# Performance work log

Hardware: AMD Instinct MI355X
Metric: run time of the kernel (lower is better)

## Reference

```python
import jax, jax.numpy as jnp
import numpy as np

# db4 reconstruction filters (pywt convention): rec_lo = reversed(dec_lo),
# rec_hi[k] = (-1)^k * dec_lo[k]
REC_LO = [0.23037781330885523, 0.7148465705525415, 0.6308807679295904,
          -0.02798376941698385, -0.18703481171888114, 0.030841381835986965,
          0.032883011666982945, -0.010597401784997278]
REC_HI = [-0.010597401784997278, -0.032883011666982945, 0.030841381835986965,
          0.18703481171888114, -0.02798376941698385, -0.6308807679295904,
          0.7148465705525415, -0.23037781330885523]
FILT_LEN = 8


def _idwt1d(cA, cD, axis):
    """Periodized single-level inverse DWT along `axis`. N -> 2N."""
    cA = jnp.moveaxis(cA, axis, -1)
    cD = jnp.moveaxis(cD, axis, -1)
    N = cA.shape[-1]
    up_a = jnp.zeros(cA.shape[:-1] + (2 * N,), cA.dtype).at[..., ::2].set(cA)
    up_d = jnp.zeros(cD.shape[:-1] + (2 * N,), cD.dtype).at[..., ::2].set(cD)
    # circular synthesis: y[m] = sum_k g[k]*up_a[m-k] + h[k]*up_d[m-k]
    y = sum(REC_LO[k] * jnp.roll(up_a, k, axis=-1) +
            REC_HI[k] * jnp.roll(up_d, k, axis=-1) for k in range(FILT_LEN))
    y = jnp.roll(y, -(FILT_LEN - 2), axis=-1)  # phase alignment (periodization)
    return jnp.moveaxis(y, -1, axis)


def setup_inputs() -> dict:
    key = jax.random.key(0)
    x = jax.random.normal(key, (64, 256, 256, 16), dtype=jnp.float32)
    return {"x": x}


def reference(x):
    # x: [B, H, W, 4*C] with channel groups = (cA, cH, cV, cD)
    c = x.shape[-1] // 4
    cA, cH, cV, cD = (x[..., :c], x[..., c:2 * c],
                      x[..., 2 * c:3 * c], x[..., 3 * c:])
    lo = _idwt1d(cA, cH, axis=1)   # [B, 2H, W, C]
    hi = _idwt1d(cV, cD, axis=1)   # [B, 2H, W, C]
    return _idwt1d(lo, hi, axis=2)  # [B, 2H, 2W, C]
```

## Files before the change

kernel.cpp:

```cpp
#include <hip/hip_runtime.h>


#define N 256
#define RJ 16
#define NC (RJ / 2)

__device__ __forceinline__ void fma4(float4& d, float s, const float4 a) {
  d.x = fmaf(s, a.x, d.x);
  d.y = fmaf(s, a.y, d.y);
  d.z = fmaf(s, a.z, d.z);
  d.w = fmaf(s, a.w, d.w);
}

__global__ __launch_bounds__(512, 4) void idwt2_sep6_kernel(
    const float* __restrict__ x, float* __restrict__ out) {
  constexpr float LO[8] = {
      0.23037781330885523f,  0.7148465705525415f,  0.6308807679295904f,
      -0.02798376941698385f, -0.18703481171888114f, 0.030841381835986965f,
      0.032883011666982945f, -0.010597401784997278f};
  constexpr float HIW[8] = {
      -0.010597401784997278f, -0.032883011666982945f, 0.030841381835986965f,
      0.18703481171888114f,  -0.02798376941698385f,  -0.6308807679295904f,
      0.7148465705525415f,   -0.23037781330885523f};
  const float Lw[2][4] = {{LO[6], LO[4], LO[2], LO[0]},
                          {LO[7], LO[5], LO[3], LO[1]}};
  const float Hw[2][4] = {{HIW[6], HIW[4], HIW[2], HIW[0]},
                          {HIW[7], HIW[5], HIW[3], HIW[1]}};

  __shared__ float4 I[2][2][2][2][N];

  const int t = threadIdx.x;
  const int bx = blockIdx.x;
  const int b = bx >> 4;
  const int r0 = (bx & 15) * RJ;

  const float4* xb = reinterpret_cast<const float4*>(x) + (size_t)b * N * N * 4;
  float4* ob = reinterpret_cast<float4*>(out) + (size_t)b * (2 * N) * (2 * N);

  const int tcol = t & (N - 1);
  const int thalf = t >> 8;
  const float4* xcolp = xb + (size_t)tcol * 4 + thalf * 2;

  float4 wA[4], wB[4], nA0, nB0, nA1, nB1;
  auto ldrow = [&](int lr, float4& A, float4& B) {
    const int gr = (r0 + lr) & (N - 1);
    A = xcolp[(size_t)gr * (N * 4)];
    B = xcolp[(size_t)gr * (N * 4) + 1];
  };

#pragma unroll
  for (int m = 0; m < 4; ++m) ldrow(m, wA[m], wB[m]);
  ldrow(4, nA0, nB0);
  ldrow(5, nA1, nB1);

  auto p1 = [&](int j, int buf, int r) {
    float4 v0 = make_float4(0.f, 0.f, 0.f, 0.f);
    float4 v1 = make_float4(0.f, 0.f, 0.f, 0.f);
#pragma unroll
    for (int sy = 0; sy < 4; ++sy) {
      const float4 a = wA[(j + sy) & 3];
      const float4 bb = wB[(j + sy) & 3];
      fma4(v0, Lw[0][sy], a);
      fma4(v0, Hw[0][sy], bb);
      fma4(v1, Lw[1][sy], a);
      fma4(v1, Hw[1][sy], bb);
    }
    I[buf][r][0][thalf][tcol] = v0;
    I[buf][r][1][thalf][tcol] = v1;
  };

  p1(0, 0, 0);
  wA[0] = nA0;
  wB[0] = nB0;
  p1(1, 0, 1);
  wA[1] = nA1;
  wB[1] = nB1;
  ldrow(6, nA0, nB0);
  ldrow(7, nA1, nB1);
  __syncthreads();

  const int jx = t >> 1;
  const int q = t & 1;
  float Lq[4], Hq[4];
#pragma unroll
  for (int s = 0; s < 4; ++s) {
    Lq[s] = q ? Lw[1][s] : Lw[0][s];
    Hq[s] = q ? Hw[1][s] : Hw[0][s];
  }

#pragma unroll 2
  for (int c = 0; c < NC; ++c) {
    const int buf = c & 1;

#pragma unroll
    for (int r = 0; r < 2; ++r) {
      float4 o0 = make_float4(0.f, 0.f, 0.f, 0.f);
      float4 o1 = make_float4(0.f, 0.f, 0.f, 0.f);
#pragma unroll
      for (int s = 0; s < 4; ++s) {
        const int xc = (jx + s) & (N - 1);
        fma4(o0, Lq[s], I[buf][r][0][0][xc]);
        fma4(o0, Hq[s], I[buf][r][0][1][xc]);
        fma4(o1, Lq[s], I[buf][r][1][0][xc]);
        fma4(o1, Hq[s], I[buf][r][1][1][xc]);
      }
      const int jy = r0 + 2 * c + r;
      float4* po = ob + (size_t)(2 * jy) * (2 * N) + t;
      po[0] = o0;
      po[2 * N] = o1;
    }

    if (c < NC - 1) {
      p1(2 * c + 2, buf ^ 1, 0);
      wA[(2 * c + 2) & 3] = nA0;
      wB[(2 * c + 2) & 3] = nB0;
      p1(2 * c + 3, buf ^ 1, 1);
      wA[(2 * c + 3) & 3] = nA1;
      wB[(2 * c + 3) & 3] = nB1;

      if (c < NC - 2) {
        ldrow(2 * c + 8, nA0, nB0);
        if (2 * c + 9 <= RJ + 2) ldrow(2 * c + 9, nA1, nB1);
      }
      __syncthreads();
    }
  }
}

extern "C" void kernel_launch(void* const* d_in, const int* in_sizes, int n_in,
                              void* d_out, int out_size, void* d_ws,
                              size_t ws_size, hipStream_t stream) {
  const float* x = reinterpret_cast<const float*>(d_in[0]);
  float* out = reinterpret_cast<float*>(d_out);
  const int grid = 64 * (N / RJ);
  idwt2_sep6_kernel<<<grid, 512, 0, stream>>>(x, out);
}
```

Before: 117.4 us.

## Process one output row pair per stage to halve LDS and raise occupancy

The column-pass loop now handles one intermediate row per iteration instead of two. This halves the shared-memory double buffer and drops one set of prefetch registers. The launch bound is raised to allow 8 waves per SIMD, so more blocks can be resident and hide memory latency better. The cost is twice as many __syncthreads barriers and a shallower per-iteration batch of independent work.

```diff
diff --git a/kernel.cpp b/kernel.cpp
--- a/kernel.cpp
+++ b/kernel.cpp
@@ -3,7 +3,6 @@
 
 #define N 256
 #define RJ 16
-#define NC (RJ / 2)
 
 __device__ __forceinline__ void fma4(float4& d, float s, const float4 a) {
   d.x = fmaf(s, a.x, d.x);
@@ -12,7 +11,7 @@
   d.w = fmaf(s, a.w, d.w);
 }
 
-__global__ __launch_bounds__(512, 4) void idwt2_sep6_kernel(
+__global__ __launch_bounds__(512, 8) void idwt2_sep7_kernel(
     const float* __restrict__ x, float* __restrict__ out) {
   constexpr float LO[8] = {
       0.23037781330885523f,  0.7148465705525415f,  0.6308807679295904f,
@@ -27,7 +26,7 @@
   const float Hw[2][4] = {{HIW[6], HIW[4], HIW[2], HIW[0]},
                           {HIW[7], HIW[5], HIW[3], HIW[1]}};
 
-  __shared__ float4 I[2][2][2][2][N];
+  __shared__ float4 I[2][2][2][N];
 
   const int t = threadIdx.x;
   const int bx = blockIdx.x;
@@ -41,19 +40,14 @@
   const int thalf = t >> 8;
   const float4* xcolp = xb + (size_t)tcol * 4 + thalf * 2;
 
-  float4 wA[4], wB[4], nA0, nB0, nA1, nB1;
+  float4 wA[4], wB[4], nA, nB;
   auto ldrow = [&](int lr, float4& A, float4& B) {
     const int gr = (r0 + lr) & (N - 1);
     A = xcolp[(size_t)gr * (N * 4)];
     B = xcolp[(size_t)gr * (N * 4) + 1];
   };
 
-#pragma unroll
-  for (int m = 0; m < 4; ++m) ldrow(m, wA[m], wB[m]);
-  ldrow(4, nA0, nB0);
-  ldrow(5, nA1, nB1);
-
-  auto p1 = [&](int j, int buf, int r) {
+  auto p1 = [&](int j, int buf) {
     float4 v0 = make_float4(0.f, 0.f, 0.f, 0.f);
     float4 v1 = make_float4(0.f, 0.f, 0.f, 0.f);
 #pragma unroll
@@ -65,18 +59,17 @@
       fma4(v1, Lw[1][sy], a);
       fma4(v1, Hw[1][sy], bb);
     }
-    I[buf][r][0][thalf][tcol] = v0;
-    I[buf][r][1][thalf][tcol] = v1;
+    I[buf][0][thalf][tcol] = v0;
+    I[buf][1][thalf][tcol] = v1;
   };
 
-  p1(0, 0, 0);
-  wA[0] = nA0;
-  wB[0] = nB0;
-  p1(1, 0, 1);
-  wA[1] = nA1;
-  wB[1] = nB1;
-  ldrow(6, nA0, nB0);
-  ldrow(7, nA1, nB1);
+#pragma unroll
+  for (int m = 0; m < 4; ++m) ldrow(m, wA[m], wB[m]);
+  ldrow(4, nA, nB);
+  p1(0, 0);
+  wA[0] = nA;
+  wB[0] = nB;
+  ldrow(5, nA, nB);
   __syncthreads();
 
   const int jx = t >> 1;
@@ -88,40 +81,32 @@
     Hq[s] = q ? Hw[1][s] : Hw[0][s];
   }
 
-#pragma unroll 2
-  for (int c = 0; c < NC; ++c) {
+#pragma unroll
+  for (int c = 0; c < RJ; ++c) {
     const int buf = c & 1;
 
+    float4 o0 = make_float4(0.f, 0.f, 0.f, 0.f);
+    float4 o1 = make_float4(0.f, 0.f, 0.f, 0.f);
 #pragma unroll
-    for (int r = 0; r < 2; ++r) {
-      float4 o0 = make_float4(0.f, 0.f, 0.f, 0.f);
-      float4 o1 = make_float4(0.f, 0.f, 0.f, 0.f);
-#pragma unroll
-      for (int s = 0; s < 4; ++s) {
-        const int xc = (jx + s) & (N - 1);
-        fma4(o0, Lq[s], I[buf][r][0][0][xc]);
-        fma4(o0, Hq[s], I[buf][r][0][1][xc]);
-        fma4(o1, Lq[s], I[buf][r][1][0][xc]);
-        fma4(o1, Hq[s], I[buf][r][1][1][xc]);
+    for (int s = 0; s < 4; ++s) {
+      const int xc = (jx + s) & (N - 1);
+      fma4(o0, Lq[s], I[buf][0][0][xc]);
+      fma4(o0, Hq[s], I[buf][0][1][xc]);
+      fma4(o1, Lq[s], I[buf][1][0][xc]);
+      fma4(o1, Hq[s], I[buf][1][1][xc]);
+    }
+    const int jy = r0 + c;
+    float4* po = ob + (size_t)(2 * jy) * (2 * N) + t;
+    po[0] = o0;
+    po[2 * N] = o1;
+
+    if (c < RJ - 1) {
+      p1(c + 1, buf ^ 1);
+      if (c <= RJ - 3) {
+        wA[(c + 1) & 3] = nA;
+        wB[(c + 1) & 3] = nB;
       }
-      const int jy = r0 + 2 * c + r;
-      float4* po = ob + (size_t)(2 * jy) * (2 * N) + t;
-      po[0] = o0;
-      po[2 * N] = o1;
-    }
-
-    if (c < NC - 1) {
-      p1(2 * c + 2, buf ^ 1, 0);
-      wA[(2 * c + 2) & 3] = nA0;
-      wB[(2 * c + 2) & 3] = nB0;
-      p1(2 * c + 3, buf ^ 1, 1);
-      wA[(2 * c + 3) & 3] = nA1;
-      wB[(2 * c + 3) & 3] = nB1;
-
-      if (c < NC - 2) {
-        ldrow(2 * c + 8, nA0, nB0);
-        if (2 * c + 9 <= RJ + 2) ldrow(2 * c + 9, nA1, nB1);
-      }
+      if (c <= RJ - 4) ldrow(c + 6, nA, nB);
       __syncthreads();
     }
   }
@@ -133,5 +118,5 @@
   const float* x = reinterpret_cast<const float*>(d_in[0]);
   float* out = reinterpret_cast<float*>(d_out);
   const int grid = 64 * (N / RJ);
-  idwt2_sep6_kernel<<<grid, 512, 0, stream>>>(x, out);
+  idwt2_sep7_kernel<<<grid, 512, 0, stream>>>(x, out);
 }
```

Measured after the change: 196.2 us. +67.1%, slower.
